# Performance work log

Measured on AMD Instinct MI355X. Metric: run time of the kernel, lower is better.

Reference implementation:

```python
import jax, jax.numpy as jnp
import numpy as np

N = 4096      # total_activities_num
D = 128       # feature dim
E = 1_000_000 # number of edges (events)
EPS = 1e-12


def setup_inputs() -> dict:
    key = jax.random.key(0)
    k1, k2, k3, k4, k5 = jax.random.split(key, 5)
    currents = jax.random.randint(k1, (E,), 0, N, dtype=jnp.int64)
    targets = jax.random.randint(k2, (E,), 0, N, dtype=jnp.int64)
    activities_features = jax.random.normal(k3, (N, D), dtype=jnp.float32)
    cases_features = jax.random.normal(k4, (E, D), dtype=jnp.float32)
    # Learned parameter W [N, N], kaiming_uniform fan_in relu -> U(-b, b), b = sqrt(6/fan_in)
    bound = float(np.sqrt(6.0 / N))
    W = jax.random.uniform(k5, (N, N), dtype=jnp.float32, minval=-bound, maxval=bound)
    return {
        "currents": currents,
        "targets": targets,
        "activities_features": activities_features,
        "cases_features": cases_features,
        "W": W,
    }


def reference(currents, targets, activities_features, cases_features, W):
    # Per-edge gather: h_emb, t_emb are [E, D]
    h_emb = activities_features[currents]
    t_emb = activities_features[targets]
    # dist = ||h + case - t||_2 per edge -> [E]
    diff = h_emb + cases_features - t_emb
    dist = jnp.sqrt(jnp.sum(diff * diff, axis=1))
    vals = jnp.exp(-dist)
    # Scatter-add into dense [N, N] attention input at (tail, head)
    att_input = jnp.zeros((N, N), dtype=activities_features.dtype)
    att_input = att_input.at[targets, currents].add(vals)
    # Row-normalize
    norm = jnp.sum(att_input, axis=1, keepdims=True)
    attention = att_input / (norm + EPS)
    # Dense GEMMs
    feat = W @ activities_features           # [N, D]
    h = attention @ feat + feat               # [N, D]
    return h
```

## Files before the change

kernel.cpp:

```cpp
#include <hip/hip_runtime.h>
#include <hip/hip_bf16.h>

typedef unsigned short u16;
typedef unsigned int   u32;

typedef __attribute__((ext_vector_type(8))) __bf16 bf16x8;
typedef __attribute__((ext_vector_type(4))) float  f32x4;
typedef __attribute__((ext_vector_type(4))) u32    u32x4;

#define NN 4096
#define DD 128
#define EPS 1e-12f

#define KS 4
#define BM 32
#define BK 128
#define KPER (NN / KS)
#define LDK 136
#define NZERO 2048

static __device__ __forceinline__ u16 f2bf(float f) {
    union { float f; u32 u; } v; v.f = f;
    u32 r = v.u + 0x7fffu + ((v.u >> 16) & 1u);
    return (u16)(r >> 16);
}
static __device__ __forceinline__ float bf2f(u16 u) {
    union { u32 i; float f; } v; v.i = (u32)u << 16; return v.f;
}

template <typename T>
static __device__ __forceinline__ auto bf2_atomic_add(T* p, T v, int)
    -> decltype(unsafeAtomicAdd(p, v), void()) {
    unsafeAtomicAdd(p, v);
}
template <typename T>
static __device__ __forceinline__ void bf2_atomic_add(T* p, T v, long) {
    u32* w = (u32*)p;
    union { u32 i; T h; } av; av.h = v;
    float alo = bf2f((u16)(av.i & 0xffff));
    float ahi = bf2f((u16)(av.i >> 16));
    u32 old = *w, assumed;
    do {
        assumed = old;
        float lo = bf2f((u16)(assumed & 0xffff)) + alo;
        float hi = bf2f((u16)(assumed >> 16)) + ahi;
        u32 nv = (u32)f2bf(lo) | ((u32)f2bf(hi) << 16);
        old = atomicCAS(w, assumed, nv);
    } while (old != assumed);
}

__global__ __launch_bounds__(256) void prep_kernel(
    const float* __restrict__ in, u16* __restrict__ out, uint4* __restrict__ attz)
{
    __shared__ __align__(16) u16 lds[128][40];
    const int t = threadIdx.x;
    if (blockIdx.x >= 128) {
        const size_t b = blockIdx.x - 128;
        uint4 z = make_uint4(0u, 0u, 0u, 0u);
#pragma unroll
        for (int i = 0; i < 4; ++i)
            attz[b * 1024 + i * 256 + t] = z;
        return;
    }
    const int k0 = blockIdx.x * 32;
#pragma unroll
    for (int i = 0; i < 4; ++i) {
        int f  = t + 256 * i;
        int kr = f >> 5;
        int n0 = (f & 31) * 4;
        float4 v = *(const float4*)(in + (size_t)(k0 + kr) * DD + n0);
        lds[n0 + 0][kr] = f2bf(v.x);
        lds[n0 + 1][kr] = f2bf(v.y);
        lds[n0 + 2][kr] = f2bf(v.z);
        lds[n0 + 3][kr] = f2bf(v.w);
    }
    __syncthreads();
    int n = t >> 1, h = t & 1;
    uint4 v0 = *(const uint4*)&lds[n][h * 16];
    uint4 v1 = *(const uint4*)&lds[n][h * 16 + 8];
    *(uint4*)(out + (size_t)n * NN + k0 + h * 16)     = v0;
    *(uint4*)(out + (size_t)n * NN + k0 + h * 16 + 8) = v1;
}

__global__ __launch_bounds__(256) void edge_kernel(
    const int* __restrict__ currents, const int* __restrict__ targets,
    const float* __restrict__ A, const float* __restrict__ cases,
    u16* __restrict__ att, int E)
{
    int e = blockIdx.x * 8 + (threadIdx.x >> 5);
    if (e >= E) return;
    int l = threadIdx.x & 31;
    int c = currents[e];
    int t = targets[e];
    f32x4 h = *(const f32x4*)(A + (size_t)c * DD + l * 4);
    f32x4 g = *(const f32x4*)(A + (size_t)t * DD + l * 4);
    f32x4 q = __builtin_nontemporal_load((const f32x4*)(cases + (size_t)e * DD + l * 4));
    f32x4 d = h + q - g;
    float s = d.x * d.x + d.y * d.y + d.z * d.z + d.w * d.w;
#pragma unroll
    for (int m = 16; m; m >>= 1) s += __shfl_xor(s, m, 64);
    if (l == 0) {
        float val = __expf(-__fsqrt_rn(s));
        u16 b = f2bf(val);
        size_t off = (size_t)t * NN + c;
        union { u32 i; __hip_bfloat162 h2; } pk;
        pk.i = (c & 1) ? ((u32)b << 16) : (u32)b;
        bf2_atomic_add((__hip_bfloat162*)(att + (off & ~(size_t)1)), pk.h2, 0);
    }
}

template<bool ROWSUM, bool ABF16>
__global__ __launch_bounds__(512, 4) void gemm_splitk(
    const void* __restrict__ AmatV,
    const u16*  __restrict__ BT,
    float* __restrict__ part,
    float* __restrict__ rsum_part)
{
    __shared__ __align__(16) u16 As[BM * LDK];
    __shared__ __align__(16) u16 Bs[DD * LDK];

    const int m0   = blockIdx.x * BM;
    const int ks   = blockIdx.y;
    const int kbeg = ks * KPER;
    const int t    = threadIdx.x;
    const int wave = t >> 6;
    const int lane = t & 63;
    const int quad = lane >> 4;
    const int l16  = lane & 15;

    const int ar = t >> 4;
    const int aq = t & 15;
    const int bn = t >> 2;
    const int bq = t & 3;

    const float* Apf = (const float*)AmatV + (size_t)(m0 + ar) * NN + kbeg + aq * 4;
    const u16*   Aph = (const u16*)AmatV   + (size_t)(m0 + ar) * NN + kbeg + aq * 8;
    const u16*   Bp  = BT + (size_t)bn * NN + kbeg + bq * 32;

    f32x4 vaA0, vaA1, vaB0, vaB1; u32x4 vahA, vahB;
    if constexpr (ABF16) {
        vahA = __builtin_nontemporal_load((const u32x4*)Aph);
        vahB = __builtin_nontemporal_load((const u32x4*)(Aph + BK));
    } else {
        vaA0 = __builtin_nontemporal_load((const f32x4*)Apf);
        vaA1 = __builtin_nontemporal_load((const f32x4*)(Apf + 64));
        vaB0 = __builtin_nontemporal_load((const f32x4*)(Apf + BK));
        vaB1 = __builtin_nontemporal_load((const f32x4*)(Apf + BK + 64));
    }
    uint4 vb0 = *(const uint4*)(Bp);
    uint4 vb1 = *(const uint4*)(Bp + 8);
    uint4 vb2 = *(const uint4*)(Bp + 16);
    uint4 vb3 = *(const uint4*)(Bp + 24);

    f32x4 acc0 = {0.f, 0.f, 0.f, 0.f};
    f32x4 acc1 = {0.f, 0.f, 0.f, 0.f};
    float rsum = 0.f;

#define STAGE_A_BF16(VAH)                                                   \
    {                                                                       \
        if (ROWSUM) {                                                       \
            _Pragma("unroll")                                               \
            for (int j = 0; j < 4; ++j) {                                   \
                u32 w = (VAH)[j];                                           \
                rsum += bf2f((u16)(w & 0xffff)) + bf2f((u16)(w >> 16));     \
            }                                                               \
        }                                                                   \
        *(u32x4*)&As[ar * LDK + aq * 8] = (VAH);                            \
    }
#define STAGE_A_F32(V0, V1)                                                 \
    {                                                                       \
        if (ROWSUM) {                                                       \
            rsum += ((V0).x + (V0).y) + ((V0).z + (V0).w)                   \
                  + ((V1).x + (V1).y) + ((V1).z + (V1).w);                  \
        }                                                                   \
        ushort4 u0, u1;                                                     \
        u0.x = f2bf((V0).x); u0.y = f2bf((V0).y);                           \
        u0.z = f2bf((V0).z); u0.w = f2bf((V0).w);                           \
        u1.x = f2bf((V1).x); u1.y = f2bf((V1).y);                           \
        u1.z = f2bf((V1).z); u1.w = f2bf((V1).w);                           \
        *(ushort4*)&As[ar * LDK + aq * 4]      = u0;                        \
        *(ushort4*)&As[ar * LDK + aq * 4 + 64] = u1;                        \
    }
#define STAGE_B()                                                           \
    {                                                                       \
        *(uint4*)&Bs[bn * LDK + bq * 32]      = vb0;                        \
        *(uint4*)&Bs[bn * LDK + bq * 32 + 8]  = vb1;                        \
        *(uint4*)&Bs[bn * LDK + bq * 32 + 16] = vb2;                        \
        *(uint4*)&Bs[bn * LDK + bq * 32 + 24] = vb3;                        \
    }
#define LOAD_B(KOFF)                                                        \
    {                                                                       \
        vb0 = *(const uint4*)(Bp + (KOFF));                                 \
        vb1 = *(const uint4*)(Bp + (KOFF) + 8);                             \
        vb2 = *(const uint4*)(Bp + (KOFF) + 16);                            \
        vb3 = *(const uint4*)(Bp + (KOFF) + 24);                            \
    }
#define MFMA_PHASE()                                                        \
    _Pragma("unroll")                                                       \
    for (int k2 = 0; k2 < 4; ++k2) {                                        \
        bf16x8 a0 = *(const bf16x8*)&As[l16 * LDK + k2 * 32 + quad * 8];    \
        bf16x8 a1 = *(const bf16x8*)&As[(16 + l16) * LDK + k2 * 32 + quad * 8]; \
        bf16x8 b  = *(const bf16x8*)&Bs[(wave * 16 + l16) * LDK + k2 * 32 + quad * 8]; \
        acc0 = __builtin_amdgcn_mfma_f32_16x16x32_bf16(a0, b, acc0, 0, 0, 0); \
        acc1 = __builtin_amdgcn_mfma_f32_16x16x32_bf16(a1, b, acc1, 0, 0, 0); \
    }

    for (int kk = 0; kk < KPER; kk += 2 * BK) {
        if constexpr (ABF16) { STAGE_A_BF16(vahA); } else { STAGE_A_F32(vaA0, vaA1); }
        STAGE_B();
        __syncthreads();
        if (kk + 2 * BK < KPER) {
            if constexpr (ABF16) {
                vahA = __builtin_nontemporal_load((const u32x4*)(Aph + kk + 2 * BK));
            } else {
                vaA0 = __builtin_nontemporal_load((const f32x4*)(Apf + kk + 2 * BK));
                vaA1 = __builtin_nontemporal_load((const f32x4*)(Apf + kk + 2 * BK + 64));
            }
        }
        LOAD_B(kk + BK);
        MFMA_PHASE();
        __syncthreads();

        if constexpr (ABF16) { STAGE_A_BF16(vahB); } else { STAGE_A_F32(vaB0, vaB1); }
        STAGE_B();
        __syncthreads();
        if (kk + 3 * BK < KPER) {
            if constexpr (ABF16) {
                vahB = __builtin_nontemporal_load((const u32x4*)(Aph + kk + 3 * BK));
            } else {
                vaB0 = __builtin_nontemporal_load((const f32x4*)(Apf + kk + 3 * BK));
                vaB1 = __builtin_nontemporal_load((const f32x4*)(Apf + kk + 3 * BK + 64));
            }
        }
        if (kk + 2 * BK < KPER) LOAD_B(kk + 2 * BK);
        MFMA_PHASE();
        __syncthreads();
    }

    float* P = part + (size_t)ks * NN * DD;
#pragma unroll
    for (int r = 0; r < 4; ++r) {
        int row0 = m0 + quad * 4 + r;
        int col  = wave * 16 + l16;
        P[(size_t)row0 * DD + col]        = acc0[r];
        P[(size_t)(row0 + 16) * DD + col] = acc1[r];
    }

    if (ROWSUM) {
#pragma unroll
        for (int m = 8; m; m >>= 1) rsum += __shfl_xor(rsum, m, 64);
        if ((t & 15) == 0) rsum_part[ks * NN + m0 + ar] = rsum;
    }
#undef STAGE_A_BF16
#undef STAGE_A_F32
#undef STAGE_B
#undef LOAD_B
#undef MFMA_PHASE
}

__global__ __launch_bounds__(256) void combine_feat_bt2(
    const float* __restrict__ part, float* __restrict__ feat,
    u16* __restrict__ BT2)
{
    __shared__ __align__(16) u16 lt[128][40];
    const int b = blockIdx.x;
    const int t = threadIdx.x;
    const int S = NN * DD / 4;
    const int base = b * 1024;
#pragma unroll
    for (int it = 0; it < 4; ++it) {
        int i = base + it * 256 + t;
        const float4* p = (const float4*)part;
        float4 a = p[i], b4 = p[i + S], c = p[i + 2 * S], d = p[i + 3 * S];
        float4 s;
        s.x = (a.x + b4.x) + (c.x + d.x);
        s.y = (a.y + b4.y) + (c.y + d.y);
        s.z = (a.z + b4.z) + (c.z + d.z);
        s.w = (a.w + b4.w) + (c.w + d.w);
        ((float4*)feat)[i] = s;
        int lrow = it * 8 + (t >> 5);
        int col0 = (i & 31) * 4;
        lt[col0 + 0][lrow] = f2bf(s.x);
        lt[col0 + 1][lrow] = f2bf(s.y);
        lt[col0 + 2][lrow] = f2bf(s.z);
        lt[col0 + 3][lrow] = f2bf(s.w);
    }
    __syncthreads();
    int col = t >> 1, half = t & 1;
    uint4 v0 = *(const uint4*)&lt[col][half * 16];
    uint4 v1 = *(const uint4*)&lt[col][half * 16 + 8];
    *(uint4*)(BT2 + (size_t)col * NN + b * 32 + half * 16)     = v0;
    *(uint4*)(BT2 + (size_t)col * NN + b * 32 + half * 16 + 8) = v1;
}

__global__ __launch_bounds__(256) void combine_out(
    const float* __restrict__ part, const float* __restrict__ rsum_part,
    const float* __restrict__ feat, float* __restrict__ out)
{
    int i = blockIdx.x * 256 + threadIdx.x;
    int row = i >> 5;
    const float4* p = (const float4*)part;
    const int S = NN * DD / 4;
    float4 a = p[i], b = p[i + S], c = p[i + 2 * S], d = p[i + 3 * S];
    float ns = (rsum_part[row] + rsum_part[row + NN])
             + (rsum_part[row + 2 * NN] + rsum_part[row + 3 * NN]);
    float sc = 1.0f / (ns + EPS);
    float4 f = ((const float4*)feat)[i];
    float4 s;
    s.x = ((a.x + b.x) + (c.x + d.x)) * sc + f.x;
    s.y = ((a.y + b.y) + (c.y + d.y)) * sc + f.y;
    s.z = ((a.z + b.z) + (c.z + d.z)) * sc + f.z;
    s.w = ((a.w + b.w) + (c.w + d.w)) * sc + f.w;
    ((float4*)out)[i] = s;
}

extern "C" void kernel_launch(void* const* d_in, const int* in_sizes, int n_in,
                              void* d_out, int out_size, void* d_ws, size_t ws_size,
                              hipStream_t stream)
{
    const int*   currents = (const int*)d_in[0];
    const int*   targets  = (const int*)d_in[1];
    const float* acts     = (const float*)d_in[2];
    const float* cases    = (const float*)d_in[3];
    const float* W        = (const float*)d_in[4];
    float*       out      = (float*)d_out;
    const int E = in_sizes[0];

    char* ws = (char*)d_ws;
    u16*   att       = (u16*)ws;
    float* part      = (float*)(ws + (size_t)NN * NN * 2);
    float* feat      = part + (size_t)KS * NN * DD;
    u16*   BT1       = (u16*)(feat + (size_t)NN * DD);
    u16*   BT2       = BT1 + (size_t)DD * NN;
    float* rsum_part = (float*)(BT2 + (size_t)DD * NN);

    prep_kernel<<<128 + NZERO, 256, 0, stream>>>(acts, BT1, (uint4*)att);

    edge_kernel<<<(E + 7) / 8, 256, 0, stream>>>(currents, targets, acts, cases,
                                                 att, E);

    gemm_splitk<false, false><<<dim3(NN / BM, KS), 512, 0, stream>>>(W, BT1, part, nullptr);
    combine_feat_bt2<<<128, 256, 0, stream>>>(part, feat, BT2);

    gemm_splitk<true, true><<<dim3(NN / BM, KS), 512, 0, stream>>>(att, BT2, part, rsum_part);
    combine_out<<<NN * DD / 4 / 256, 256, 0, stream>>>(part, rsum_part, feat, out);
}
```

Measured before the change: 185.6 us.

## Fuse GEMM chain into one cooperative kernel with grid-wide syncs

Replaces the four back-end launches (W GEMM, combine/transposition, attention GEMM, final combine) with a single cooperative kernel of 512 blocks that separates the stages with grid.sync(). The aim is to remove the launch gaps and tail drain between dependent kernels. A fallback path launches the original four kernels if the cooperative launch fails. The cost is the grid barriers themselves, and stages that use only some of the blocks (the 128-block combine) leave the rest idle.

```diff
diff --git a/kernel.cpp b/kernel.cpp
--- a/kernel.cpp
+++ b/kernel.cpp
@@ -1,5 +1,8 @@
 #include <hip/hip_runtime.h>
 #include <hip/hip_bf16.h>
+#include <hip/hip_cooperative_groups.h>
+
+namespace cg = cooperative_groups;
 
 typedef unsigned short u16;
 typedef unsigned int   u32;
@@ -110,17 +113,14 @@
 }
 
 template<bool ROWSUM, bool ABF16>
-__global__ __launch_bounds__(512, 4) void gemm_splitk(
-    const void* __restrict__ AmatV,
-    const u16*  __restrict__ BT,
-    float* __restrict__ part,
-    float* __restrict__ rsum_part)
-{
-    __shared__ __align__(16) u16 As[BM * LDK];
-    __shared__ __align__(16) u16 Bs[DD * LDK];
-
-    const int m0   = blockIdx.x * BM;
-    const int ks   = blockIdx.y;
+static __device__ __forceinline__ void gemm_body(
+    const void* __restrict__ AmatV, const u16* __restrict__ BT,
+    float* __restrict__ part, float* __restrict__ rsum_part,
+    u16* As, u16* Bs)
+{
+    const int bid  = blockIdx.x;
+    const int m0   = (bid & 127) * BM;
+    const int ks   = bid >> 7;
     const int kbeg = ks * KPER;
     const int t    = threadIdx.x;
     const int wave = t >> 6;
@@ -258,42 +258,100 @@
 #undef MFMA_PHASE
 }
 
-__global__ __launch_bounds__(256) void combine_feat_bt2(
+static __device__ __forceinline__ void combine_bt2_body(
     const float* __restrict__ part, float* __restrict__ feat,
-    u16* __restrict__ BT2)
-{
-    __shared__ __align__(16) u16 lt[128][40];
+    u16* __restrict__ BT2, u16* ltraw)
+{
+    u16 (*lt)[40] = (u16(*)[40])ltraw;
     const int b = blockIdx.x;
     const int t = threadIdx.x;
     const int S = NN * DD / 4;
     const int base = b * 1024;
-#pragma unroll
-    for (int it = 0; it < 4; ++it) {
-        int i = base + it * 256 + t;
+    if (t < 256) {
+#pragma unroll
+        for (int it = 0; it < 4; ++it) {
+            int i = base + it * 256 + t;
+            const float4* p = (const float4*)part;
+            float4 a = p[i], b4 = p[i + S], c = p[i + 2 * S], d = p[i + 3 * S];
+            float4 s;
+            s.x = (a.x + b4.x) + (c.x + d.x);
+            s.y = (a.y + b4.y) + (c.y + d.y);
+            s.z = (a.z + b4.z) + (c.z + d.z);
+            s.w = (a.w + b4.w) + (c.w + d.w);
+            ((float4*)feat)[i] = s;
+            int lrow = it * 8 + (t >> 5);
+            int col0 = (i & 31) * 4;
+            lt[col0 + 0][lrow] = f2bf(s.x);
+            lt[col0 + 1][lrow] = f2bf(s.y);
+            lt[col0 + 2][lrow] = f2bf(s.z);
+            lt[col0 + 3][lrow] = f2bf(s.w);
+        }
+    }
+    __syncthreads();
+    if (t < 256) {
+        int col = t >> 1, half = t & 1;
+        uint4 v0 = *(const uint4*)&lt[col][half * 16];
+        uint4 v1 = *(const uint4*)&lt[col][half * 16 + 8];
+        *(uint4*)(BT2 + (size_t)col * NN + b * 32 + half * 16)     = v0;
+        *(uint4*)(BT2 + (size_t)col * NN + b * 32 + half * 16 + 8) = v1;
+    }
+}
+
+__global__ __launch_bounds__(512, 4) void back_chain(
+    const float* __restrict__ W,   const u16* __restrict__ BT1,
+    const u16* __restrict__ att,   u16* __restrict__ BT2,
+    float* __restrict__ part,      float* __restrict__ rsum_part,
+    float* __restrict__ feat,      float* __restrict__ out)
+{
+    __shared__ __align__(16) u16 As[BM * LDK];
+    __shared__ __align__(16) u16 Bs[DD * LDK];
+    cg::grid_group grid = cg::this_grid();
+
+    gemm_body<false, false>(W, BT1, part, nullptr, As, Bs);
+    grid.sync();
+
+    if (blockIdx.x < 128) combine_bt2_body(part, feat, BT2, Bs);
+    grid.sync();
+
+    gemm_body<true, true>(att, BT2, part, rsum_part, As, Bs);
+    grid.sync();
+
+    if (threadIdx.x < 256) {
+        int i = blockIdx.x * 256 + threadIdx.x;
+        int row = i >> 5;
         const float4* p = (const float4*)part;
-        float4 a = p[i], b4 = p[i + S], c = p[i + 2 * S], d = p[i + 3 * S];
+        const int S = NN * DD / 4;
+        float4 a = p[i], b = p[i + S], c = p[i + 2 * S], d = p[i + 3 * S];
+        float ns = (rsum_part[row] + rsum_part[row + NN])
+                 + (rsum_part[row + 2 * NN] + rsum_part[row + 3 * NN]);
+        float sc = 1.0f / (ns + EPS);
+        float4 f = ((const float4*)feat)[i];
         float4 s;
-        s.x = (a.x + b4.x) + (c.x + d.x);
-        s.y = (a.y + b4.y) + (c.y + d.y);
-        s.z = (a.z + b4.z) + (c.z + d.z);
-        s.w = (a.w + b4.w) + (c.w + d.w);
-        ((float4*)feat)[i] = s;
-        int lrow = it * 8 + (t >> 5);
-        int col0 = (i & 31) * 4;
-        lt[col0 + 0][lrow] = f2bf(s.x);
-        lt[col0 + 1][lrow] = f2bf(s.y);
-        lt[col0 + 2][lrow] = f2bf(s.z);
-        lt[col0 + 3][lrow] = f2bf(s.w);
-    }
-    __syncthreads();
-    int col = t >> 1, half = t & 1;
-    uint4 v0 = *(const uint4*)&lt[col][half * 16];
-    uint4 v1 = *(const uint4*)&lt[col][half * 16 + 8];
-    *(uint4*)(BT2 + (size_t)col * NN + b * 32 + half * 16)     = v0;
-    *(uint4*)(BT2 + (size_t)col * NN + b * 32 + half * 16 + 8) = v1;
-}
-
-__global__ __launch_bounds__(256) void combine_out(
+        s.x = ((a.x + b.x) + (c.x + d.x)) * sc + f.x;
+        s.y = ((a.y + b.y) + (c.y + d.y)) * sc + f.y;
+        s.z = ((a.z + b.z) + (c.z + d.z)) * sc + f.z;
+        s.w = ((a.w + b.w) + (c.w + d.w)) * sc + f.w;
+        ((float4*)out)[i] = s;
+    }
+}
+
+template<bool ROWSUM, bool ABF16>
+__global__ __launch_bounds__(512, 4) void gemm_splitk_fb(
+    const void* __restrict__ AmatV, const u16* __restrict__ BT,
+    float* __restrict__ part, float* __restrict__ rsum_part)
+{
+    __shared__ __align__(16) u16 As[BM * LDK];
+    __shared__ __align__(16) u16 Bs[DD * LDK];
+    gemm_body<ROWSUM, ABF16>(AmatV, BT, part, rsum_part, As, Bs);
+}
+__global__ __launch_bounds__(512) void combine_bt2_fb(
+    const float* __restrict__ part, float* __restrict__ feat,
+    u16* __restrict__ BT2)
+{
+    __shared__ __align__(16) u16 Bs[DD * LDK];
+    combine_bt2_body(part, feat, BT2, Bs);
+}
+__global__ __launch_bounds__(256) void combine_out_fb(
     const float* __restrict__ part, const float* __restrict__ rsum_part,
     const float* __restrict__ feat, float* __restrict__ out)
 {
@@ -339,9 +397,17 @@
     edge_kernel<<<(E + 7) / 8, 256, 0, stream>>>(currents, targets, acts, cases,
                                                  att, E);
 
-    gemm_splitk<false, false><<<dim3(NN / BM, KS), 512, 0, stream>>>(W, BT1, part, nullptr);
-    combine_feat_bt2<<<128, 256, 0, stream>>>(part, feat, BT2);
-
-    gemm_splitk<true, true><<<dim3(NN / BM, KS), 512, 0, stream>>>(att, BT2, part, rsum_part);
-    combine_out<<<NN * DD / 4 / 256, 256, 0, stream>>>(part, rsum_part, feat, out);
-}
+    const float* Wa = W; const u16* BT1a = BT1; const u16* atta = att;
+    u16* BT2a = BT2; float* parta = part; float* rsa = rsum_part;
+    float* feata = feat; float* outa = out;
+    void* args[] = { (void*)&Wa, (void*)&BT1a, (void*)&atta, (void*)&BT2a,
+                     (void*)&parta, (void*)&rsa, (void*)&feata, (void*)&outa };
+    hipError_t err = hipLaunchCooperativeKernel(
+        (const void*)back_chain, dim3(512), dim3(512), args, 0, stream);
+    if (err != hipSuccess) {
+        gemm_splitk_fb<false, false><<<512, 512, 0, stream>>>(W, BT1, part, nullptr);
+        combine_bt2_fb<<<128, 512, 0, stream>>>(part, feat, BT2);
+        gemm_splitk_fb<true, true><<<512, 512, 0, stream>>>(att, BT2, part, rsum_part);
+        combine_out_fb<<<NN * DD / 4 / 256, 256, 0, stream>>>(part, rsum_part, feat, out);
+    }
+}
```

Result: slower. 373.7 us (+101.3%).
